# Kernel optimization log

Measured on AMD Instinct MI355X. Metric: run time of the kernel, lower is better.

The kernel has to match this reference:

```python
import jax, jax.numpy as jnp
import numpy as np

B, Cin, Cout, H, W = 8, 64, 128, 128, 128
K, S, P = 3, 1, 1
KK = K * K
EPS = 1e-5


def _conv2d(x, w, b=None):
    out = jax.lax.conv_general_dilated(
        x, w, window_strides=(S, S), padding=[(P, P), (P, P)],
        dimension_numbers=('NCHW', 'OIHW', 'NCHW'))
    if b is not None:
        out = out + b[None, :, None, None]
    return out


def setup_inputs() -> dict:
    key = jax.random.key(0)
    k = jax.random.split(key, 5)
    sc = 1.0 / np.sqrt(Cin * KK)
    return {
        'x': jax.random.normal(k[0], (B, Cin, H, W), jnp.float32),
        'offset_w': jax.random.normal(k[1], (2 * KK, Cin, K, K), jnp.float32) * sc,
        'offset_b': jnp.zeros((2 * KK,), jnp.float32),
        'mask_w': jax.random.normal(k[2], (KK, Cin, K, K), jnp.float32) * sc,
        'mask_b': jnp.zeros((KK,), jnp.float32),
        'conv_w': jax.random.normal(k[3], (Cout, Cin, K, K), jnp.float32) * sc,
    }


def _deform_conv2d(x, offset, mask, w):
    """Modulated deformable conv (torchvision deform_conv2d semantics)."""
    Bn, C, Hh, Ww = x.shape
    Ho, Wo = offset.shape[2], offset.shape[3]
    off = offset.reshape(Bn, KK, 2, Ho, Wo)  # (y, x) pairs per kernel tap
    ky, kx = jnp.meshgrid(jnp.arange(K), jnp.arange(K), indexing='ij')
    ky = ky.reshape(KK).astype(x.dtype)
    kx = kx.reshape(KK).astype(x.dtype)
    hy = (jnp.arange(Ho) * S - P).astype(x.dtype)
    wx = (jnp.arange(Wo) * S - P).astype(x.dtype)
    # sampling positions [B, KK, Ho, Wo]
    py = off[:, :, 0] + ky[None, :, None, None] + hy[None, None, :, None]
    px = off[:, :, 1] + kx[None, :, None, None] + wx[None, None, None, :]

    y0 = jnp.floor(py)
    x0 = jnp.floor(px)
    wy1 = py - y0; wx1 = px - x0
    wy0 = 1.0 - wy1; wx0 = 1.0 - wx1

    xf = x.reshape(Bn, C, Hh * Ww)

    def gather(yi, xi):
        valid = ((yi >= 0) & (yi < Hh) & (xi >= 0) & (xi < Ww)).astype(x.dtype)
        yc = jnp.clip(yi, 0, Hh - 1).astype(jnp.int32)
        xc = jnp.clip(xi, 0, Ww - 1).astype(jnp.int32)
        idx = (yc * Ww + xc).reshape(Bn, -1)  # [B, KK*Ho*Wo]
        vals = jnp.take_along_axis(xf, idx[:, None, :], axis=2)  # [B, C, KK*Ho*Wo]
        return vals.reshape(Bn, C, KK, Ho, Wo) * valid.reshape(Bn, 1, KK, Ho, Wo)

    v = (gather(y0, x0) * (wy0 * wx0)[:, None]
         + gather(y0, x0 + 1) * (wy0 * wx1)[:, None]
         + gather(y0 + 1, x0) * (wy1 * wx0)[:, None]
         + gather(y0 + 1, x0 + 1) * (wy1 * wx1)[:, None])  # [B, C, KK, Ho, Wo]
    v = v * mask[:, None]  # modulation
    return jnp.einsum('bckhw,ock->bohw', v, w.reshape(w.shape[0], C, KK))


def reference(x, offset_w, offset_b, mask_w, mask_b, conv_w):
    offset = _conv2d(x, offset_w, offset_b)
    mask = jax.nn.sigmoid(_conv2d(x, mask_w, mask_b))
    out = _deform_conv2d(x, offset, mask, conv_w)
    # BatchNorm2d(affine=False), training-mode normalization over (N, H, W)
    mean = out.mean(axis=(0, 2, 3), keepdims=True)
    var = out.var(axis=(0, 2, 3), keepdims=True)
    return jax.nn.relu((out - mean) * jax.lax.rsqrt(var + EPS))
```

## Files before the change

### kernel.cpp

```cpp
#include <hip/hip_runtime.h>
#include <hip/hip_bf16.h>

#define H_ 128
#define W_ 128
#define HW 16384
#define CIN 64
#define COUT 128
#define KK9 9
#define BATCH 8
#define NPIX (BATCH * HW)
#define KDIM 576

typedef short bf16x8 __attribute__((ext_vector_type(8)));
typedef float f32x4  __attribute__((ext_vector_type(4)));
typedef unsigned short ushort_t;

union U4B { uint4 u; bf16x8 v; };

__device__ __forceinline__ float us2f(unsigned short u) {
    unsigned int v = ((unsigned int)u) << 16;
    float f;
    __builtin_memcpy(&f, &v, 4);
    return f;
}
__device__ __forceinline__ float lo_f(unsigned int w) {
    unsigned int v = w << 16;
    float f;
    __builtin_memcpy(&f, &v, 4);
    return f;
}
__device__ __forceinline__ float hi_f(unsigned int w) {
    unsigned int v = w & 0xffff0000u;
    float f;
    __builtin_memcpy(&f, &v, 4);
    return f;
}
__device__ __forceinline__ unsigned short f2us_bf(float f) {
    __hip_bfloat16 h = __float2bfloat16(f);
    unsigned short u;
    __builtin_memcpy(&u, &h, 2);
    return u;
}
__device__ __forceinline__ unsigned int pack2(float a, float b) {
    return (unsigned int)f2us_bf(a) | ((unsigned int)f2us_bf(b) << 16);
}

template <bool F32>
__device__ __forceinline__ float ld_in(const void* p, long i) {
    if (F32) return ((const float*)p)[i];
    return us2f(((const unsigned short*)p)[i]);
}

__global__ void detect_zero(const uint4* __restrict__ xr4,
                            float* __restrict__ flag,
                            float* __restrict__ gstat) {
    int t = threadIdx.x;
#pragma unroll
    for (int i = 0; i < 16; ++i) gstat[i * 256 + t] = 0.0f;
    if (t < 64) {
        uint4 v = xr4[t];
        unsigned int w[4] = {v.x, v.y, v.z, v.w};
        int big = 0;
#pragma unroll
        for (int q = 0; q < 4; ++q) {
            big += (((w[q] >> 7)  & 0xFF) >= 0xC0);
            big += (((w[q] >> 23) & 0xFF) >= 0xC0);
        }
        unsigned long long m = __ballot(big > 0);
        if (t == 0) flag[0] = m ? 1.0f : 0.0f;
    }
}

template <bool F32>
__device__ __forceinline__ void prep_body(const void* offw, const void* offb,
                                          const void* maskw, const void* maskb,
                                          const void* convw,
                                          ushort_t* wTs, ushort_t* wcats,
                                          float* bias, int i) {
    if (i < 73728) {
        int j = i & 7, lane = (i >> 3) & 63, n = (i >> 9) & 7, ks = i >> 12;
        int co = n * 16 + (lane & 15);
        int k  = ks * 32 + ((lane >> 4) << 3) + j;
        int kk = k >> 6, ci = k & 63;
        wTs[i] = f2us_bf(ld_in<F32>(convw, (long)co * KDIM + ci * 9 + kk));
    } else if (i < 73728 + 18432) {
        int i2 = i - 73728;
        int j = i2 & 7, lane = (i2 >> 3) & 63, n = (i2 >> 9) & 1, ks = i2 >> 10;
        int co2 = n * 16 + (lane & 15);
        int k   = ks * 32 + ((lane >> 4) << 3) + j;
        int kk = k >> 6, ci = k & 63;
        float v = 0.0f;
        if (co2 < 18)      v = ld_in<F32>(offw,  (long)co2 * KDIM + ci * 9 + kk);
        else if (co2 < 27) v = ld_in<F32>(maskw, (long)(co2 - 18) * KDIM + ci * 9 + kk);
        wcats[i2] = f2us_bf(v);
    } else if (i < 73728 + 18432 + 32) {
        int j = i - 73728 - 18432;
        float v = 0.0f;
        if (j < 18)      v = ld_in<F32>(offb, j);
        else if (j < 27) v = ld_in<F32>(maskb, j - 18);
        bias[j] = v;
    }
}

__global__ void prep_weights(const void* __restrict__ offw,
                             const void* __restrict__ offb,
                             const void* __restrict__ maskw,
                             const void* __restrict__ maskb,
                             const void* __restrict__ convw,
                             const float* __restrict__ flag,
                             ushort_t* __restrict__ wTs,
                             ushort_t* __restrict__ wcats,
                             float* __restrict__ bias) {
    int i = blockIdx.x * 256 + threadIdx.x;
    if (flag[0] != 0.0f)
        prep_body<true>(offw, offb, maskw, maskb, convw, wTs, wcats, bias, i);
    else
        prep_body<false>(offw, offb, maskw, maskb, convw, wTs, wcats, bias, i);
}

template <bool F32>
__device__ __forceinline__ void transpose_body(const void* x, ushort_t* xnb) {
    __shared__ float tile[CIN * 65];
    int blk  = blockIdx.x;
    int b    = blk >> 8;
    int pix0 = (blk & 255) * 64;
    int t    = threadIdx.x;
#pragma unroll
    for (int pass = 0; pass < 4; ++pass) {
        int slot = pass * 256 + t;
        int ci = slot >> 4;
        int f4 = slot & 15;
        long base = (long)(b * CIN + ci) * HW + pix0 + f4 * 4;
        float v0, v1, v2, v3;
        if (F32) {
            float4 v = *(const float4*)((const float*)x + base);
            v0 = v.x; v1 = v.y; v2 = v.z; v3 = v.w;
        } else {
            ushort4 u = *(const ushort4*)((const ushort_t*)x + base);
            v0 = us2f(u.x); v1 = us2f(u.y); v2 = us2f(u.z); v3 = us2f(u.w);
        }
        tile[ci * 65 + f4 * 4 + 0] = v0;
        tile[ci * 65 + f4 * 4 + 1] = v1;
        tile[ci * 65 + f4 * 4 + 2] = v2;
        tile[ci * 65 + f4 * 4 + 3] = v3;
    }
    __syncthreads();
#pragma unroll
    for (int pass = 0; pass < 4; ++pass) {
        int slot = pass * 256 + t;
        int px = slot >> 4;
        int c4 = slot & 15;
        ushort4 o;
        o.x = f2us_bf(tile[(c4 * 4 + 0) * 65 + px]);
        o.y = f2us_bf(tile[(c4 * 4 + 1) * 65 + px]);
        o.z = f2us_bf(tile[(c4 * 4 + 2) * 65 + px]);
        o.w = f2us_bf(tile[(c4 * 4 + 3) * 65 + px]);
        *(ushort4*)(xnb + (size_t)(b * HW + pix0 + px) * CIN + c4 * 4) = o;
    }
}

__global__ __launch_bounds__(256) void transpose_x(const void* __restrict__ x,
                                                   const float* __restrict__ flag,
                                                   ushort_t* __restrict__ xnb) {
    if (flag[0] != 0.0f) transpose_body<true>(x, xnb);
    else                 transpose_body<false>(x, xnb);
}

__device__ __forceinline__ void compute_tap(int yp_t, int xp_t,
                                            float oy, float ox, float mk,
                                            int* ofs, float* wg) {
    float py  = (float)yp_t + oy;
    float pxf = (float)xp_t + ox;
    float y0f = floorf(py), x0f = floorf(pxf);
    int yi = (int)y0f, xi = (int)x0f;
    float wy1 = py - y0f, wx1 = pxf - x0f;
    float wy0 = 1.0f - wy1, wx0 = 1.0f - wx1;
    int ya  = min(max(yi, 0), H_ - 1);
    int yb  = min(max(yi + 1, 0), H_ - 1);
    int xa  = min(max(xi, 0), W_ - 1);
    int xb2 = min(max(xi + 1, 0), W_ - 1);
    bool vy0 = (yi >= 0) & (yi < H_);
    bool vy1 = (yi >= -1) & (yi < H_ - 1);
    bool vx0 = (xi >= 0) & (xi < W_);
    bool vx1 = (xi >= -1) & (xi < W_ - 1);
    float m0 = mk * wy0, m1 = mk * wy1;
    wg[0] = (vy0 & vx0) ? m0 * wx0 : 0.0f;
    wg[1] = (vy0 & vx1) ? m0 * wx1 : 0.0f;
    wg[2] = (vy1 & vx0) ? m1 * wx0 : 0.0f;
    wg[3] = (vy1 & vx1) ? m1 * wx1 : 0.0f;
    int ra = ya << 13, rb = yb << 13;
    int ca = xa << 6,  cb_ = xb2 << 6;
    ofs[0] = ra + ca;  ofs[1] = ra + cb_;
    ofs[2] = rb + ca;  ofs[3] = rb + cb_;
}

__device__ __forceinline__ void issue_half(const ushort_t* __restrict__ xb,
                                           const int* ofs, int hoff, uint4* cb) {
#pragma unroll
    for (int c = 0; c < 4; ++c)
        cb[c] = *(const uint4*)(xb + ofs[c] + hoff);
}

__device__ __forceinline__ void consume_half(int slot, const uint4* cb,
                                             const float* wg,
                                             const ushort_t* __restrict__ ldsB,
                                             int lane, f32x4* acc) {
    float2 v2[4];
#pragma unroll
    for (int j = 0; j < 4; ++j) v2[j] = make_float2(0.f, 0.f);
#pragma unroll
    for (int c = 0; c < 4; ++c) {
        float w = wg[c];
        unsigned int ww[4] = {cb[c].x, cb[c].y, cb[c].z, cb[c].w};
#pragma unroll
        for (int j = 0; j < 4; ++j) {
            v2[j].x = fmaf(w, lo_f(ww[j]), v2[j].x);
            v2[j].y = fmaf(w, hi_f(ww[j]), v2[j].y);
        }
    }
    U4B a;
    a.u = make_uint4(pack2(v2[0].x, v2[0].y), pack2(v2[1].x, v2[1].y),
                     pack2(v2[2].x, v2[2].y), pack2(v2[3].x, v2[3].y));
    const ushort_t* bbase = ldsB + ((size_t)(slot * 8) * 64 + lane) * 8;
    __builtin_amdgcn_s_setprio(1);
#pragma unroll
    for (int n = 0; n < 8; ++n) {
        bf16x8 bf = *(const bf16x8*)(bbase + n * 64 * 8);
        acc[n] = __builtin_amdgcn_mfma_f32_16x16x32_bf16(a.v, bf, acc[n], 0, 0, 0);
    }
    __builtin_amdgcn_s_setprio(0);
}

__global__ __launch_bounds__(1024, 4) void fused_conv_deform(
        const ushort_t* __restrict__ xnb,
        const ushort_t* __restrict__ wcats,
        const float* __restrict__ bias,
        const ushort_t* __restrict__ wTs,
        ushort_t* __restrict__ prebn,
        float* __restrict__ gstat) {
    __shared__ uint4 lds[8192];

    float2* offL  = (float2*)(lds + 6400);
    float*  maskS = (float*) (lds + 7552);
    float*  red   = (float*) (lds + 8128);

    int t    = threadIdx.x;
    int bid  = blockIdx.x;
    int sbid = (bid & 7) * 64 + (bid >> 3);
    int pix0 = sbid * 256;
    int b    = pix0 >> 14;
    int rem0 = pix0 & 16383;
    int y0   = rem0 >> 7;

    const uint4* wc4 = (const uint4*)wcats;
    for (int i = t; i < 2304; i += 1024) lds[i] = wc4[i];
    const uint4* xrow4 = (const uint4*)(xnb + (size_t)b * HW * CIN);
    int sxq = t >> 3, sc16 = t & 7;
#pragma unroll
    for (int r = 0; r < 4; ++r) {
        int gy = y0 - 1 + r;
        if (gy >= 0 && gy < H_) {
            uint4 v = xrow4[(size_t)gy * 1024 + t];
            lds[2304 + r * 1024 + sxq * 8 + (sc16 ^ (sxq & 7))] = v;
        }
    }
    if (t < 256) red[t] = 0.0f;
    __syncthreads();

    int wave = t >> 6, lane = t & 63, mrow = lane & 15, quad = lane >> 4;
    int px_l = wave * 16 + mrow;

    {
        int ly = px_l >> 7;
        int xp = px_l & 127;
        uint4 af0[9], af1[9];
#pragma unroll
        for (int kk = 0; kk < 9; ++kk) {
            int ty = kk / 3, tx = kk % 3;
            int tr = ly + ty;
            int gy = y0 - 1 + tr;
            int xq = xp + tx - 1;
            bool ok = (gy >= 0) && (gy < H_) && (xq >= 0) && (xq < W_);
            int xc = min(max(xq, 0), W_ - 1);
            int base = 2304 + tr * 1024 + xc * 8;
            uint4 a0 = lds[base + ((quad    ) ^ (xc & 7))];
            uint4 a1 = lds[base + ((quad + 4) ^ (xc & 7))];
            af0[kk] = ok ? a0 : make_uint4(0, 0, 0, 0);
            af1[kk] = ok ? a1 : make_uint4(0, 0, 0, 0);
        }
        f32x4 cacc[2];
        cacc[0] = (f32x4){0.f, 0.f, 0.f, 0.f};
        cacc[1] = (f32x4){0.f, 0.f, 0.f, 0.f};
        const ushort_t* ldsBc = (const ushort_t*)lds;
#pragma unroll
        for (int kk = 0; kk < 9; ++kk) {
#pragma unroll
            for (int half = 0; half < 2; ++half) {
                int ks = kk * 2 + half;
                U4B a; a.u = half ? af1[kk] : af0[kk];
#pragma unroll
                for (int n = 0; n < 2; ++n) {
                    bf16x8 bf = *(const bf16x8*)(ldsBc + ((ks * 2 + n) * 64 + lane) * 8);
                    cacc[n] = __builtin_amdgcn_mfma_f32_16x16x32_bf16(a.v, bf, cacc[n], 0, 0, 0);
                }
            }
        }
#pragma unroll
        for (int n = 0; n < 2; ++n) {
            int co2 = n * 16 + mrow;
            if (co2 >= 27) continue;
            float bs = bias[co2];
#pragma unroll
            for (int r = 0; r < 4; ++r) {
                int px = wave * 16 + quad * 4 + r;
                float v = cacc[n][r] + bs;
                if (co2 < 18)
                    ((float*)offL)[((co2 >> 1) * 256 + px) * 2 + (co2 & 1)] = v;
                else
                    maskS[(co2 - 18) * 256 + px] = 1.0f / (1.0f + __expf(-v));
            }
        }
    }
    __syncthreads();

    const uint4* ws4 = (const uint4*)wTs;
    for (int i = t; i < 4608; i += 1024) lds[i] = ws4[i];

    int remp = rem0 + px_l;
    int yp  = remp >> 7, xp2 = remp & 127;
    const ushort_t* xb = xnb + (size_t)b * HW * CIN + quad * 8;

    f32x4 acc[8];
#pragma unroll
    for (int n = 0; n < 8; ++n) acc[n] = (f32x4){0.f, 0.f, 0.f, 0.f};

    int   ofs[2][4];
    float wg[2][4];
    uint4 cb[3][4];

    float2 oE  = offL[px_l];           float mkE = maskS[px_l];
    float2 oO  = offL[256 + px_l];     float mkO = maskS[256 + px_l];
    compute_tap(yp - 1, xp2 - 1, oE.x, oE.y, mkE, ofs[0], wg[0]);
    issue_half(xb, ofs[0], 0,  cb[0]);
    issue_half(xb, ofs[0], 32, cb[1]);
    oE = offL[2 * 256 + px_l];  mkE = maskS[2 * 256 + px_l];
    __builtin_amdgcn_sched_barrier(0);
    __syncthreads();

    const ushort_t* ldsB = (const ushort_t*)lds;

#pragma unroll
    for (int hs = 0; hs < 9; ++hs) {
        const int hs2 = hs + 2;
        {
            const int kk2 = hs2 >> 1;
            const int s2  = hs2 % 3;
            if ((hs2 & 1) == 0) {
                const int tp2 = kk2 & 1;
                float ooy = tp2 ? oO.x : oE.x;
                float oox = tp2 ? oO.y : oE.y;
                float omk = tp2 ? mkO  : mkE;
                compute_tap(yp + kk2 / 3 - 1, xp2 + kk2 % 3 - 1, ooy, oox, omk,
                            ofs[tp2], wg[tp2]);
                issue_half(xb, ofs[tp2], 0, cb[s2]);
                if (kk2 + 2 <= 8) {
                    float2 o = offL[(kk2 + 2) * 256 + px_l];
                    float  m = maskS[(kk2 + 2) * 256 + px_l];
                    if (tp2) { oO = o; mkO = m; } else { oE = o; mkE = m; }
                }
            } else {
                issue_half(xb, ofs[kk2 & 1], 32, cb[s2]);
            }
        }
        __builtin_amdgcn_sched_barrier(0);
        consume_half(hs, cb[hs % 3], wg[(hs >> 1) & 1], ldsB, lane, acc);
    }
    __syncthreads();
    for (int i = t; i < 4608; i += 1024) lds[i] = ws4[4608 + i];
    __syncthreads();

#pragma unroll
    for (int hs = 9; hs < 18; ++hs) {
        const int hs2 = hs + 2;
        if (hs2 < 18) {
            const int kk2 = hs2 >> 1;
            const int s2  = hs2 % 3;
            if ((hs2 & 1) == 0) {
                const int tp2 = kk2 & 1;
                float ooy = tp2 ? oO.x : oE.x;
                float oox = tp2 ? oO.y : oE.y;
                float omk = tp2 ? mkO  : mkE;
                compute_tap(yp + kk2 / 3 - 1, xp2 + kk2 % 3 - 1, ooy, oox, omk,
                            ofs[tp2], wg[tp2]);
                issue_half(xb, ofs[tp2], 0, cb[s2]);
                if (kk2 + 2 <= 8) {
                    float2 o = offL[(kk2 + 2) * 256 + px_l];
                    float  m = maskS[(kk2 + 2) * 256 + px_l];
                    if (tp2) { oO = o; mkO = m; } else { oE = o; mkE = m; }
                }
            } else {
                issue_half(xb, ofs[kk2 & 1], 32, cb[s2]);
            }
        }
        __builtin_amdgcn_sched_barrier(0);
        consume_half(hs - 9, cb[hs % 3], wg[(hs >> 1) & 1], ldsB, lane, acc);
    }

#pragma unroll
    for (int n = 0; n < 8; ++n) {
        int co = n * 16 + mrow;
        float s = 0.f, ss = 0.f;
#pragma unroll
        for (int r = 0; r < 4; ++r) {
            int pg = pix0 + wave * 16 + quad * 4 + r;
            float v = acc[n][r];
            prebn[(size_t)pg * COUT + co] = f2us_bf(v);
            s += v;
            ss += v * v;
        }
        s  += __shfl_xor(s, 16, 64);
        s  += __shfl_xor(s, 32, 64);
        ss += __shfl_xor(ss, 16, 64);
        ss += __shfl_xor(ss, 32, 64);
        if (quad == 0) {
            atomicAdd(&red[co], s);
            atomicAdd(&red[128 + co], ss);
        }
    }
    __syncthreads();
    if (t < 256) atomicAdd(&gstat[(bid & 15) * 256 + t], red[t]);
}

__global__ __launch_bounds__(256) void bn_apply_t(const ushort_t* __restrict__ prebn,
                                                  const float* __restrict__ gstat,
                                                  float* __restrict__ out) {
    __shared__ float tile[128 * 65];
    __shared__ float mvs[256];
    int t = threadIdx.x;
    if (t < 128) {
        float s = 0.f, ss = 0.f;
#pragma unroll
        for (int part = 0; part < 16; ++part) {
            s  += gstat[part * 256 + t];
            ss += gstat[part * 256 + 128 + t];
        }
        const float invN = 1.0f / (float)NPIX;
        float mean = s * invN;
        float var  = ss * invN - mean * mean;
        if (!isfinite(mean)) mean = 0.0f;
        float r = rsqrtf(fmaxf(var, 0.0f) + 1e-5f);
        if (!isfinite(r)) r = 1.0f;
        mvs[t]       = mean;
        mvs[128 + t] = r;
    }
    __syncthreads();
    int pix0 = blockIdx.x * 64;
    int b    = pix0 >> 14;
    int rem0 = pix0 & 16383;
    const uint4* src4 = (const uint4*)(prebn + (size_t)pix0 * COUT);
#pragma unroll
    for (int r = 0; r < 4; ++r) {
        int i  = r * 256 + t;
        uint4 v = src4[i];
        int p  = i >> 4;
        int c0 = (i & 15) * 8;
        unsigned int w[4] = {v.x, v.y, v.z, v.w};
#pragma unroll
        for (int j = 0; j < 4; ++j) {
            int c = c0 + j * 2;
            float f0 = lo_f(w[j]);
            float f1 = hi_f(w[j]);
            tile[c * 65 + p]       = fmaxf((f0 - mvs[c])     * mvs[128 + c],     0.0f);
            tile[(c + 1) * 65 + p] = fmaxf((f1 - mvs[c + 1]) * mvs[128 + c + 1], 0.0f);
        }
    }
    __syncthreads();
#pragma unroll
    for (int r = 0; r < 8; ++r) {
        int i  = r * 256 + t;
        int c2 = i >> 4;
        int q  = (i & 15) * 4;
        float4 w4 = make_float4(tile[c2 * 65 + q],     tile[c2 * 65 + q + 1],
                                tile[c2 * 65 + q + 2], tile[c2 * 65 + q + 3]);
        *(float4*)(out + (size_t)(b * COUT + c2) * HW + rem0 + q) = w4;
    }
}

extern "C" void kernel_launch(void* const* d_in, const int* in_sizes, int n_in,
                              void* d_out, int out_size, void* d_ws, size_t ws_size,
                              hipStream_t stream) {
    (void)in_sizes; (void)n_in; (void)out_size; (void)ws_size;
    const void* x     = d_in[0];
    const void* offw  = d_in[1];
    const void* offb  = d_in[2];
    const void* maskw = d_in[3];
    const void* maskb = d_in[4];
    const void* convw = d_in[5];

    float* ws       = (float*)d_ws;
    float* off2     = ws;
    float* mask_ws  = off2 + 2359296;
    float* bias     = mask_ws + 1179648;
    float* gstat    = bias + 32;
    float* flag     = gstat + 4096;
    ushort_t* wTs   = (ushort_t*)(flag + 16);
    ushort_t* wcats = wTs + 73728;
    ushort_t* xnb   = wcats + 18432;
    ushort_t* prebn = xnb + 8388608;
    float* out      = (float*)d_out;

    detect_zero<<<1, 256, 0, stream>>>((const uint4*)x, flag, gstat);
    prep_weights<<<361, 256, 0, stream>>>(offw, offb, maskw, maskb, convw, flag, wTs, wcats, bias);
    transpose_x<<<2048, 256, 0, stream>>>(x, flag, xnb);
    fused_conv_deform<<<512, 1024, 0, stream>>>(xnb, wcats, bias, wTs, prebn, gstat);
    bn_apply_t<<<2048, 256, 0, stream>>>(prebn, gstat, out);
}
```

Baseline: 202.0 us.

## Halve fused block size, load conv taps from global, stage weights in thirds

Shrinks the fused conv/deform block from 1024 to 512 threads covering 128 pixels (one row) and doubles the grid. The offset/mask conv taps now come straight from global memory instead of a staged 4-row LDS halo. The deform weight staging is split into three LDS passes instead of two. LDS use drops from 128KB to about 64KB so more blocks can be resident per CU, at the cost of more barriers, more weight reloads per pixel, and uncoalesced-ish global tap loads.

Result: slower. 217.2 us (+7.5%).

```diff
diff --git a/kernel.cpp b/kernel.cpp
--- a/kernel.cpp
+++ b/kernel.cpp
@@ -231,63 +231,48 @@
     __builtin_amdgcn_s_setprio(0);
 }
 
-__global__ __launch_bounds__(1024, 4) void fused_conv_deform(
+__global__ __launch_bounds__(512, 4) void fused_conv_deform(
         const ushort_t* __restrict__ xnb,
         const ushort_t* __restrict__ wcats,
         const float* __restrict__ bias,
         const ushort_t* __restrict__ wTs,
         ushort_t* __restrict__ prebn,
         float* __restrict__ gstat) {
-    __shared__ uint4 lds[8192];
-
-    float2* offL  = (float2*)(lds + 6400);
-    float*  maskS = (float*) (lds + 7552);
-    float*  red   = (float*) (lds + 8128);
+    __shared__ uint4 lds[4000];
+    float2* offL  = (float2*)(lds + 3072);
+    float*  maskS = (float*) (lds + 3648);
+    float*  red   = (float*) (lds + 3936);
 
     int t    = threadIdx.x;
     int bid  = blockIdx.x;
-    int sbid = (bid & 7) * 64 + (bid >> 3);
-    int pix0 = sbid * 256;
+    int sbid = (bid & 7) * 128 + (bid >> 3);
+    int pix0 = sbid * 128;
     int b    = pix0 >> 14;
     int rem0 = pix0 & 16383;
     int y0   = rem0 >> 7;
 
     const uint4* wc4 = (const uint4*)wcats;
-    for (int i = t; i < 2304; i += 1024) lds[i] = wc4[i];
-    const uint4* xrow4 = (const uint4*)(xnb + (size_t)b * HW * CIN);
-    int sxq = t >> 3, sc16 = t & 7;
-#pragma unroll
-    for (int r = 0; r < 4; ++r) {
-        int gy = y0 - 1 + r;
-        if (gy >= 0 && gy < H_) {
-            uint4 v = xrow4[(size_t)gy * 1024 + t];
-            lds[2304 + r * 1024 + sxq * 8 + (sc16 ^ (sxq & 7))] = v;
-        }
-    }
+    for (int i = t; i < 2304; i += 512) lds[i] = wc4[i];
     if (t < 256) red[t] = 0.0f;
-    __syncthreads();
 
     int wave = t >> 6, lane = t & 63, mrow = lane & 15, quad = lane >> 4;
     int px_l = wave * 16 + mrow;
+    int xp   = px_l;
+    const ushort_t* xb = xnb + (size_t)b * HW * CIN + quad * 8;
+
+    uint4 af0[9], af1[9];
+#pragma unroll
+    for (int kk = 0; kk < 9; ++kk) {
+        int yy = y0 + kk / 3 - 1;
+        int xq = xp + kk % 3 - 1;
+        bool ok = (yy >= 0) && (yy < H_) && (xq >= 0) && (xq < W_);
+        const ushort_t* src = xb + (size_t)(yy * W_ + xq) * CIN;
+        af0[kk] = ok ? *(const uint4*)src        : make_uint4(0, 0, 0, 0);
+        af1[kk] = ok ? *(const uint4*)(src + 32) : make_uint4(0, 0, 0, 0);
+    }
+    __syncthreads();
 
     {
-        int ly = px_l >> 7;
-        int xp = px_l & 127;
-        uint4 af0[9], af1[9];
-#pragma unroll
-        for (int kk = 0; kk < 9; ++kk) {
-            int ty = kk / 3, tx = kk % 3;
-            int tr = ly + ty;
-            int gy = y0 - 1 + tr;
-            int xq = xp + tx - 1;
-            bool ok = (gy >= 0) && (gy < H_) && (xq >= 0) && (xq < W_);
-            int xc = min(max(xq, 0), W_ - 1);
-            int base = 2304 + tr * 1024 + xc * 8;
-            uint4 a0 = lds[base + ((quad    ) ^ (xc & 7))];
-            uint4 a1 = lds[base + ((quad + 4) ^ (xc & 7))];
-            af0[kk] = ok ? a0 : make_uint4(0, 0, 0, 0);
-            af1[kk] = ok ? a1 : make_uint4(0, 0, 0, 0);
-        }
         f32x4 cacc[2];
         cacc[0] = (f32x4){0.f, 0.f, 0.f, 0.f};
         cacc[1] = (f32x4){0.f, 0.f, 0.f, 0.f};
@@ -315,20 +300,19 @@
                 int px = wave * 16 + quad * 4 + r;
                 float v = cacc[n][r] + bs;
                 if (co2 < 18)
-                    ((float*)offL)[((co2 >> 1) * 256 + px) * 2 + (co2 & 1)] = v;
+                    ((float*)offL)[((co2 >> 1) * 128 + px) * 2 + (co2 & 1)] = v;
                 else
-                    maskS[(co2 - 18) * 256 + px] = 1.0f / (1.0f + __expf(-v));
+                    maskS[(co2 - 18) * 128 + px] = 1.0f / (1.0f + __expf(-v));
             }
         }
     }
     __syncthreads();
 
     const uint4* ws4 = (const uint4*)wTs;
-    for (int i = t; i < 4608; i += 1024) lds[i] = ws4[i];
+    for (int i = t; i < 3072; i += 512) lds[i] = ws4[i];
 
     int remp = rem0 + px_l;
     int yp  = remp >> 7, xp2 = remp & 127;
-    const ushort_t* xb = xnb + (size_t)b * HW * CIN + quad * 8;
 
     f32x4 acc[8];
 #pragma unroll
@@ -339,72 +323,63 @@
     uint4 cb[3][4];
 
     float2 oE  = offL[px_l];           float mkE = maskS[px_l];
-    float2 oO  = offL[256 + px_l];     float mkO = maskS[256 + px_l];
+    float2 oO  = offL[128 + px_l];     float mkO = maskS[128 + px_l];
     compute_tap(yp - 1, xp2 - 1, oE.x, oE.y, mkE, ofs[0], wg[0]);
     issue_half(xb, ofs[0], 0,  cb[0]);
     issue_half(xb, ofs[0], 32, cb[1]);
-    oE = offL[2 * 256 + px_l];  mkE = maskS[2 * 256 + px_l];
+    oE = offL[2 * 128 + px_l];  mkE = maskS[2 * 128 + px_l];
     __builtin_amdgcn_sched_barrier(0);
     __syncthreads();
 
     const ushort_t* ldsB = (const ushort_t*)lds;
 
-#pragma unroll
-    for (int hs = 0; hs < 9; ++hs) {
-        const int hs2 = hs + 2;
-        {
-            const int kk2 = hs2 >> 1;
-            const int s2  = hs2 % 3;
-            if ((hs2 & 1) == 0) {
-                const int tp2 = kk2 & 1;
-                float ooy = tp2 ? oO.x : oE.x;
-                float oox = tp2 ? oO.y : oE.y;
-                float omk = tp2 ? mkO  : mkE;
-                compute_tap(yp + kk2 / 3 - 1, xp2 + kk2 % 3 - 1, ooy, oox, omk,
-                            ofs[tp2], wg[tp2]);
-                issue_half(xb, ofs[tp2], 0, cb[s2]);
-                if (kk2 + 2 <= 8) {
-                    float2 o = offL[(kk2 + 2) * 256 + px_l];
-                    float  m = maskS[(kk2 + 2) * 256 + px_l];
-                    if (tp2) { oO = o; mkO = m; } else { oE = o; mkE = m; }
-                }
-            } else {
-                issue_half(xb, ofs[kk2 & 1], 32, cb[s2]);
-            }
-        }
-        __builtin_amdgcn_sched_barrier(0);
+#define ISSUE_STEP(hs)  do {                                                  \
+    const int hs2 = (hs) + 2;                                                 \
+    if (hs2 < 18) {                                                           \
+        const int kk2 = hs2 >> 1;                                             \
+        const int s2  = hs2 % 3;                                              \
+        if ((hs2 & 1) == 0) {                                                 \
+            const int tp2 = kk2 & 1;                                          \
+            float ooy = tp2 ? oO.x : oE.x;                                    \
+            float oox = tp2 ? oO.y : oE.y;                                    \
+            float omk = tp2 ? mkO  : mkE;                                     \
+            compute_tap(yp + kk2 / 3 - 1, xp2 + kk2 % 3 - 1, ooy, oox, omk,   \
+                        ofs[tp2], wg[tp2]);                                   \
+            issue_half(xb, ofs[tp2], 0, cb[s2]);                              \
+            if (kk2 + 2 <= 8) {                                               \
+                float2 o = offL[(kk2 + 2) * 128 + px_l];                      \
+                float  m = maskS[(kk2 + 2) * 128 + px_l];                     \
+                if (tp2) { oO = o; mkO = m; } else { oE = o; mkE = m; }       \
+            }                                                                 \
+        } else {                                                              \
+            issue_half(xb, ofs[kk2 & 1], 32, cb[s2]);                         \
+        }                                                                     \
+    }                                                                         \
+    __builtin_amdgcn_sched_barrier(0);                                        \
+} while (0)
+
+#pragma unroll
+    for (int hs = 0; hs < 6; ++hs) {
+        ISSUE_STEP(hs);
         consume_half(hs, cb[hs % 3], wg[(hs >> 1) & 1], ldsB, lane, acc);
     }
     __syncthreads();
-    for (int i = t; i < 4608; i += 1024) lds[i] = ws4[4608 + i];
-    __syncthreads();
-
-#pragma unroll
-    for (int hs = 9; hs < 18; ++hs) {
-        const int hs2 = hs + 2;
-        if (hs2 < 18) {
-            const int kk2 = hs2 >> 1;
-            const int s2  = hs2 % 3;
-            if ((hs2 & 1) == 0) {
-                const int tp2 = kk2 & 1;
-                float ooy = tp2 ? oO.x : oE.x;
-                float oox = tp2 ? oO.y : oE.y;
-                float omk = tp2 ? mkO  : mkE;
-                compute_tap(yp + kk2 / 3 - 1, xp2 + kk2 % 3 - 1, ooy, oox, omk,
-                            ofs[tp2], wg[tp2]);
-                issue_half(xb, ofs[tp2], 0, cb[s2]);
-                if (kk2 + 2 <= 8) {
-                    float2 o = offL[(kk2 + 2) * 256 + px_l];
-                    float  m = maskS[(kk2 + 2) * 256 + px_l];
-                    if (tp2) { oO = o; mkO = m; } else { oE = o; mkE = m; }
-                }
-            } else {
-                issue_half(xb, ofs[kk2 & 1], 32, cb[s2]);
-            }
-        }
-        __builtin_amdgcn_sched_barrier(0);
-        consume_half(hs - 9, cb[hs % 3], wg[(hs >> 1) & 1], ldsB, lane, acc);
-    }
+    for (int i = t; i < 3072; i += 512) lds[i] = ws4[3072 + i];
+    __syncthreads();
+#pragma unroll
+    for (int hs = 6; hs < 12; ++hs) {
+        ISSUE_STEP(hs);
+        consume_half(hs - 6, cb[hs % 3], wg[(hs >> 1) & 1], ldsB, lane, acc);
+    }
+    __syncthreads();
+    for (int i = t; i < 3072; i += 512) lds[i] = ws4[6144 + i];
+    __syncthreads();
+#pragma unroll
+    for (int hs = 12; hs < 18; ++hs) {
+        ISSUE_STEP(hs);
+        consume_half(hs - 12, cb[hs % 3], wg[(hs >> 1) & 1], ldsB, lane, acc);
+    }
+#undef ISSUE_STEP
 
 #pragma unroll
     for (int n = 0; n < 8; ++n) {
@@ -512,6 +487,6 @@
     detect_zero<<<1, 256, 0, stream>>>((const uint4*)x, flag, gstat);
     prep_weights<<<361, 256, 0, stream>>>(offw, offb, maskw, maskb, convw, flag, wTs, wcats, bias);
     transpose_x<<<2048, 256, 0, stream>>>(x, flag, xnb);
-    fused_conv_deform<<<512, 1024, 0, stream>>>(xnb, wcats, bias, wTs, prebn, gstat);
+    fused_conv_deform<<<1024, 512, 0, stream>>>(xnb, wcats, bias, wTs, prebn, gstat);
     bn_apply_t<<<2048, 256, 0, stream>>>(prebn, gstat, out);
 }
```
